# Kernel optimization log

Measured on AMD Instinct MI355X. Metric: run time of the kernel, lower is better.

Reference implementation:

```python
import jax, jax.numpy as jnp
import numpy as np

COL_IDX = 5  # colIdx: column used as sort key
REVERSE = False


def setup_inputs() -> dict:
    key = jax.random.key(0)
    # x: [batch, seq, feat]
    x = jax.random.normal(key, (32, 4096, 256), dtype=jnp.float32)
    return {"x": x}


def reference(x):
    # tf.nn.top_k(x[:, :, nc], k=S) returns indices of a full descending sort
    # with stable tie-breaking (earlier index first). jnp.argsort is stable,
    # so argsort of the negated key reproduces it exactly.
    keys = x[:, :, COL_IDX]                       # [B, S]
    idxs = jnp.argsort(-keys, axis=1)             # [B, S] descending order
    if REVERSE:
        idxs = idxs[:, ::-1]
    # gather_nd with (batch, idx) pairs == take_along_axis over the seq dim
    return jnp.take_along_axis(x, idxs[:, :, None], axis=1)  # [B, S, F]
```

## Files before the change

### kernel.cpp

```cpp
#include <hip/hip_runtime.h>
#include <stdint.h>

#define BATCH   32
#define ROWS    4096
#define COLS    256
#define COL_IDX 5

typedef unsigned long long u64;
typedef unsigned int       u32;

__global__ __launch_bounds__(256)
void extract_keys_kernel(const float* __restrict__ x, u64* __restrict__ keys) {
    const int i = blockIdx.x * 256 + threadIdx.x;
    u32 u = __float_as_uint(x[(size_t)i * COLS + COL_IDX]);
    u = (u >> 31) ? ~u : (u | 0x80000000u);
    u = ~u;
    keys[i] = ((u64)u << 32) | (u32)(i & (ROWS - 1));
}

__global__ __launch_bounds__(256, 8)
void rank_copy_kernel(const float* __restrict__ x,
                      const u64* __restrict__ keys,
                      float* __restrict__ out) {
    __shared__ int part[4][64];
    const int w    = (int)threadIdx.x >> 6;
    const int lane = (int)threadIdx.x & 63;
    const int b    = blockIdx.x >> 6;
    const int r0   = (blockIdx.x & 63) << 6;
    const u64* __restrict__ kb = keys + (size_t)b * ROWS;

    const u64 my = kb[r0 + lane];
    int rank = 0;
    const int jbeg = w * (ROWS / 4);
    for (int j0 = jbeg; j0 < jbeg + ROWS / 4; j0 += 64) {
        const u64 kv = kb[j0 + lane];
        const u32 lo = (u32)kv, hi = (u32)(kv >> 32);
        #pragma unroll
        for (int l = 0; l < 64; ++l) {
            const u32 klo = (u32)__builtin_amdgcn_readlane(lo, l);
            const u32 khi = (u32)__builtin_amdgcn_readlane(hi, l);
            const u64 kk  = ((u64)khi << 32) | klo;
            rank += (kk < my) ? 1 : 0;
        }
    }
    part[w][lane] = rank;
    __syncthreads();
    const int total = part[0][lane] + part[1][lane]
                    + part[2][lane] + part[3][lane];

    const float4* __restrict__ src  =
        (const float4*)(x + ((size_t)b * ROWS + r0) * COLS);
    float4* __restrict__ outb = (float4*)(out + (size_t)b * ROWS * COLS);
    #pragma unroll 4
    for (int t = 0; t < 16; ++t) {
        const int l   = w * 16 + t;
        const int dst = __builtin_amdgcn_readlane(total, l);
        outb[(size_t)dst * 64 + lane] = src[(size_t)l * 64 + lane];
    }
}

extern "C" void kernel_launch(void* const* d_in, const int* in_sizes, int n_in,
                              void* d_out, int out_size, void* d_ws, size_t ws_size,
                              hipStream_t stream) {
    const float* x   = (const float*)d_in[0];
    float*       out = (float*)d_out;
    u64*         keys = (u64*)d_ws;

    extract_keys_kernel<<<(BATCH * ROWS) / 256, 256, 0, stream>>>(x, keys);
    rank_copy_kernel<<<BATCH * 64, 256, 0, stream>>>(x, keys, out);
}
```

Measured before the change: 248.5 us.

## Prefetch rows into registers and rank keys via wave ballot-popcount

The 16 float4 row chunks each thread copies are now loaded into registers before the ranking work, so their memory latency overlaps with the compare loop. Ranking is inverted: each of the 64 query keys is broadcast in turn and compared against 16 register-held keys per lane, with ballot plus popcount counting matches across the wave. This replaces the per-key readlane-and-compare inner loop with fewer scalar broadcasts and vector compares. Register pressure rises, so the occupancy hint drops from 8 to 4 blocks per CU.

```diff
diff --git a/kernel.cpp b/kernel.cpp
--- a/kernel.cpp
+++ b/kernel.cpp
@@ -18,7 +18,7 @@
     keys[i] = ((u64)u << 32) | (u32)(i & (ROWS - 1));
 }
 
-__global__ __launch_bounds__(256, 8)
+__global__ __launch_bounds__(256, 4)
 void rank_copy_kernel(const float* __restrict__ x,
                       const u64* __restrict__ keys,
                       float* __restrict__ out) {
@@ -29,33 +29,45 @@
     const int r0   = (blockIdx.x & 63) << 6;
     const u64* __restrict__ kb = keys + (size_t)b * ROWS;
 
-    const u64 my = kb[r0 + lane];
-    int rank = 0;
+    const float4* __restrict__ src =
+        (const float4*)(x + ((size_t)b * ROWS + r0) * COLS);
+    float4 d[16];
+    #pragma unroll
+    for (int t = 0; t < 16; ++t)
+        d[t] = src[(size_t)(w * 16 + t) * 64 + lane];
+
     const int jbeg = w * (ROWS / 4);
-    for (int j0 = jbeg; j0 < jbeg + ROWS / 4; j0 += 64) {
-        const u64 kv = kb[j0 + lane];
-        const u32 lo = (u32)kv, hi = (u32)(kv >> 32);
+    u64 kv[16];
+    #pragma unroll
+    for (int t = 0; t < 16; ++t)
+        kv[t] = kb[jbeg + t * 64 + lane];
+
+    const u64 my    = kb[r0 + lane];
+    const u32 my_lo = (u32)my, my_hi = (u32)(my >> 32);
+
+    int vrank = 0;
+    #pragma unroll 2
+    for (int m = 0; m < 64; ++m) {
+        const u32 klo = (u32)__builtin_amdgcn_readlane((int)my_lo, m);
+        const u32 khi = (u32)__builtin_amdgcn_readlane((int)my_hi, m);
+        const u64 mym = ((u64)khi << 32) | klo;
+        int rank_m = 0;
         #pragma unroll
-        for (int l = 0; l < 64; ++l) {
-            const u32 klo = (u32)__builtin_amdgcn_readlane(lo, l);
-            const u32 khi = (u32)__builtin_amdgcn_readlane(hi, l);
-            const u64 kk  = ((u64)khi << 32) | klo;
-            rank += (kk < my) ? 1 : 0;
-        }
+        for (int t = 0; t < 16; ++t)
+            rank_m += (int)__popcll(__ballot(kv[t] < mym));
+        vrank = (lane == m) ? rank_m : vrank;
     }
-    part[w][lane] = rank;
+
+    part[w][lane] = vrank;
     __syncthreads();
     const int total = part[0][lane] + part[1][lane]
                     + part[2][lane] + part[3][lane];
 
-    const float4* __restrict__ src  =
-        (const float4*)(x + ((size_t)b * ROWS + r0) * COLS);
     float4* __restrict__ outb = (float4*)(out + (size_t)b * ROWS * COLS);
-    #pragma unroll 4
+    #pragma unroll
     for (int t = 0; t < 16; ++t) {
-        const int l   = w * 16 + t;
-        const int dst = __builtin_amdgcn_readlane(total, l);
-        outb[(size_t)dst * 64 + lane] = src[(size_t)l * 64 + lane];
+        const int dst = __builtin_amdgcn_readlane(total, w * 16 + t);
+        outb[(size_t)dst * 64 + lane] = d[t];
     }
 }
 
```

Result: slower. 276.1 us (+11.1%).
